# Kernel optimization log

Measured on AMD Instinct MI355X. Metric: run time of the kernel, lower is better.

## Reference

```python
import jax, jax.numpy as jnp
import numpy as np

EMBED = 256; HEADS = 8; LEVELS = 1; POINTS = 4; QUEUE = 2
HB = 200; WB = 200; NQ = HB * WB; BS = 1


def bilinear_sample(img, grid, h, w):
    # img: (BH, D, h*w) flattened feature map; grid: (BH, N, 2) in [-1, 1]
    # torch.grid_sample(align_corners=False, padding_mode='zeros') semantics
    gx, gy = grid[..., 0], grid[..., 1]
    x = (gx + 1.0) * (w * 0.5) - 0.5
    y = (gy + 1.0) * (h * 0.5) - 0.5
    x0 = jnp.floor(x); y0 = jnp.floor(y)
    lx = x - x0; ly = y - y0
    x0i = x0.astype(jnp.int32); y0i = y0.astype(jnp.int32)

    def corner(xi, yi, wgt):
        valid = ((xi >= 0) & (xi < w) & (yi >= 0) & (yi < h)).astype(img.dtype)
        idx = jnp.clip(yi, 0, h - 1) * w + jnp.clip(xi, 0, w - 1)  # (BH, N)
        vals = jax.vmap(lambda im, ix: im[:, ix])(img, idx)  # (BH, D, N)
        return vals * (wgt * valid)[:, None, :]

    return (corner(x0i, y0i, (1 - lx) * (1 - ly))
            + corner(x0i + 1, y0i, lx * (1 - ly))
            + corner(x0i, y0i + 1, (1 - lx) * ly)
            + corner(x0i + 1, y0i + 1, lx * ly))


def ms_deform_attn(value, shapes, loc, aw):
    # value: (B, Nv, H, D); loc: (B, nq, H, L, P, 2); aw: (B, nq, H, L, P)
    B, Nv, H, D = value.shape
    nq = loc.shape[1]; P = loc.shape[4]
    grids = 2.0 * loc - 1.0
    start = 0
    per_level = []
    for l in range(shapes.shape[0]):
        h, w = int(shapes[l, 0]), int(shapes[l, 1])
        vl = value[:, start:start + h * w].reshape(B, h, w, H, D)
        vl = vl.transpose(0, 3, 4, 1, 2).reshape(B * H, D, h * w)
        g = grids[:, :, :, l].transpose(0, 2, 1, 3, 4).reshape(B * H, nq * P, 2)
        samp = bilinear_sample(vl, g, h, w).reshape(B, H, D, nq, P)
        per_level.append(samp)
        start += h * w
    sampled = jnp.stack(per_level, axis=4)  # (B, H, D, nq, L, P)
    w_ = aw.transpose(0, 2, 1, 3, 4)[:, :, None]  # (B, H, 1, nq, L, P)
    out = (sampled * w_).sum(axis=(-1, -2))  # (B, H, D, nq)
    return out.reshape(B, H * D, nq).transpose(0, 2, 1)  # (B, nq, E)


def setup_inputs():
    key = jax.random.key(0)
    ks = jax.random.split(key, 10)
    s = 0.02
    n_off = QUEUE * HEADS * LEVELS * POINTS * 2
    n_aw = QUEUE * HEADS * LEVELS * POINTS
    return {
        "query": jax.random.normal(ks[0], (BS, NQ, EMBED), jnp.float32),
        "query_pos": jax.random.normal(ks[1], (BS, NQ, EMBED), jnp.float32),
        "value": jax.random.normal(ks[2], (BS * QUEUE, NQ, EMBED), jnp.float32),
        "reference_points": jax.random.uniform(ks[3], (BS * QUEUE, NQ, LEVELS, 2), jnp.float32),
        "spatial_shapes": jnp.array([[HB, WB]], dtype=jnp.int32),
        "W_off": jax.random.normal(ks[4], (EMBED * QUEUE, n_off), jnp.float32) * s,
        "b_off": jnp.zeros((n_off,), jnp.float32),
        "W_attn": jax.random.normal(ks[5], (EMBED * QUEUE, n_aw), jnp.float32) * s,
        "b_attn": jnp.zeros((n_aw,), jnp.float32),
        "W_val": jax.random.normal(ks[6], (EMBED, EMBED), jnp.float32) * s,
        "b_val": jnp.zeros((EMBED,), jnp.float32),
        "W_out": jax.random.normal(ks[7], (EMBED, EMBED), jnp.float32) * s,
        "b_out": jnp.zeros((EMBED,), jnp.float32),
    }


def reference(query, query_pos, value, reference_points, spatial_shapes,
              W_off, b_off, W_attn, b_attn, W_val, b_val, W_out, b_out):
    shapes = np.asarray(spatial_shapes)  # static level shapes
    bs, nq, E = query.shape
    identity = query
    q = query + query_pos
    # temporal query: concat current-frame value with query
    q2 = jnp.concatenate([value[:bs], q], axis=-1)  # (bs, nq, 2E)
    v = value @ W_val + b_val  # (bs*2, nv, E)
    nv = v.shape[1]
    v = v.reshape(bs * QUEUE, nv, HEADS, E // HEADS)
    off = (q2 @ W_off + b_off).reshape(bs, nq, HEADS, QUEUE, LEVELS, POINTS, 2)
    aw = (q2 @ W_attn + b_attn).reshape(bs, nq, HEADS, QUEUE, LEVELS * POINTS)
    aw = jax.nn.softmax(aw, axis=-1).reshape(bs, nq, HEADS, QUEUE, LEVELS, POINTS)
    aw = aw.transpose(0, 3, 1, 2, 4, 5).reshape(bs * QUEUE, nq, HEADS, LEVELS, POINTS)
    off = off.transpose(0, 3, 1, 2, 4, 5, 6).reshape(bs * QUEUE, nq, HEADS, LEVELS, POINTS, 2)
    # normalized sampling locations: (bs*2, nq, H, L, P, 2)
    normalizer = jnp.stack([spatial_shapes[..., 1], spatial_shapes[..., 0]], -1).astype(jnp.float32)
    loc = reference_points[:, :, None, :, None, :] + off / normalizer[None, None, None, :, None, :]
    out = ms_deform_attn(v, shapes, loc, aw)  # (bs*2, nq, E)
    # average over the BEV queue (current + history)
    out = out.transpose(1, 2, 0).reshape(nq, E, bs, QUEUE).mean(-1).transpose(2, 0, 1)
    out = out @ W_out + b_out
    return out + identity
```

## Files before the change

### kernel.cpp

```cpp
#include <hip/hip_runtime.h>
#include <math.h>

#define NQ    40000
#define EMB   256
#define NHEAD 8
#define HDIM  32
#define HB    200
#define WB    200
#define NCOL  192
#define HPIX  2560000

typedef __attribute__((ext_vector_type(8))) __bf16 bf16x8;
typedef __attribute__((ext_vector_type(4))) float f32x4;

static __device__ __forceinline__ unsigned short f2bf(float f) {
  unsigned u = __float_as_uint(f);
  u = u + 0x7fffu + ((u >> 16) & 1u);
  return (unsigned short)(u >> 16);
}
static __device__ __forceinline__ float bf2f(unsigned short s) {
  return __uint_as_float(((unsigned)s) << 16);
}
static __device__ __forceinline__ void accp(float4& lo4, float4& hi4, uint4 u, float w) {
  lo4.x += w * __uint_as_float(u.x << 16);
  lo4.y += w * __uint_as_float(u.x & 0xffff0000u);
  lo4.z += w * __uint_as_float(u.y << 16);
  lo4.w += w * __uint_as_float(u.y & 0xffff0000u);
  hi4.x += w * __uint_as_float(u.z << 16);
  hi4.y += w * __uint_as_float(u.z & 0xffff0000u);
  hi4.z += w * __uint_as_float(u.w << 16);
  hi4.w += w * __uint_as_float(u.w & 0xffff0000u);
}

__global__ __launch_bounds__(256) void conv_w(
    const float* __restrict__ W_off, const float* __restrict__ b_off,
    const float* __restrict__ W_attn, const float* __restrict__ b_attn,
    const float* __restrict__ W_val, const float* __restrict__ W_out,
    unsigned short* __restrict__ Wc1t, unsigned short* __restrict__ Wvt,
    unsigned short* __restrict__ Wot, float* __restrict__ bc1)
{
  int idx = blockIdx.x * 256 + threadIdx.x;
  if (idx < 65536) {
    int k = idx >> 7, n = idx & 127;
    Wc1t[(size_t)n * 512 + k] = f2bf(W_off[idx]);
  } else if (idx < 98304) {
    int j = idx - 65536;
    int k = j >> 6, n = j & 63;
    Wc1t[(size_t)(128 + n) * 512 + k] = f2bf(W_attn[j]);
  } else if (idx < 163840) {
    int j = idx - 98304;
    int k = j >> 8, n = j & 255;
    Wvt[(size_t)n * 256 + k] = f2bf(W_val[j]);
  } else if (idx < 229376) {
    int j = idx - 163840;
    int k = j >> 8, n = j & 255;
    Wot[(size_t)n * 256 + k] = f2bf(W_out[j]);
  } else if (idx < 229568) {
    int n = idx - 229376;
    bc1[n] = (n < 128) ? b_off[n] : b_attn[n - 128];
  }
}

template<int K, int N, int AMODE, int OMODE, bool RESID>
static __device__ __forceinline__ void gemm_body(
    int bx, char* lds,
    const void* __restrict__ Aptr, const void* __restrict__ Aq2a,
    const void* __restrict__ Aq2b, const unsigned short* __restrict__ Bt,
    const float* __restrict__ bias, const float* __restrict__ resid,
    void* __restrict__ outp)
{
  constexpr int NFR = N / 64;
  constexpr int NP  = N + 8;
  unsigned short* trn = (unsigned short*)lds;

  const int t = threadIdx.x;
  const int m0 = bx * 32;
  const int wid = t >> 6, lane = t & 63;
  const int wn = wid * (N / 4);
  const int lr = lane & 15, quad = lane >> 4;

  auto cvt_store = [&](int r, int c, float4 f0, float4 f1) {
    union { unsigned short us[8]; uint4 v; } u;
    u.us[0] = f2bf(f0.x); u.us[1] = f2bf(f0.y);
    u.us[2] = f2bf(f0.z); u.us[3] = f2bf(f0.w);
    u.us[4] = f2bf(f1.x); u.us[5] = f2bf(f1.y);
    u.us[6] = f2bf(f1.z); u.us[7] = f2bf(f1.w);
    *(uint4*)(lds + (size_t)r * 512 + ((c ^ (r & 7)) * 16)) = u.v;
  };

  auto stage_h = [&](int hh) {
    const int c = t & 31, r0 = t >> 5;
    if (AMODE == 1 || hh == 0) {
      float4 f[4][2];
      #pragma unroll
      for (int l = 0; l < 4; l++) {
        const float* s = (const float*)Aptr
            + (size_t)(m0 + r0 + 8 * l) * 256 + c * 8;
        f[l][0] = *(const float4*)s; f[l][1] = *(const float4*)(s + 4);
      }
      #pragma unroll
      for (int l = 0; l < 4; l++)
        cvt_store(r0 + 8 * l, c, f[l][0], f[l][1]);
    } else {
      float4 fq[4][2], fp[4][2];
      #pragma unroll
      for (int l = 0; l < 4; l++) {
        int row = m0 + r0 + 8 * l;
        const float* sq = (const float*)Aq2a + (size_t)row * 256 + c * 8;
        const float* sp = (const float*)Aq2b + (size_t)row * 256 + c * 8;
        fq[l][0] = *(const float4*)sq; fq[l][1] = *(const float4*)(sq + 4);
        fp[l][0] = *(const float4*)sp; fp[l][1] = *(const float4*)(sp + 4);
      }
      #pragma unroll
      for (int l = 0; l < 4; l++) {
        float4 f0 = make_float4(fq[l][0].x + fp[l][0].x, fq[l][0].y + fp[l][0].y,
                                fq[l][0].z + fp[l][0].z, fq[l][0].w + fp[l][0].w);
        float4 f1 = make_float4(fq[l][1].x + fp[l][1].x, fq[l][1].y + fp[l][1].y,
                                fq[l][1].z + fp[l][1].z, fq[l][1].w + fp[l][1].w);
        cvt_store(r0 + 8 * l, c, f0, f1);
      }
    }
  };

  f32x4 acc[2][NFR];
  #pragma unroll
  for (int i = 0; i < 2; i++)
    #pragma unroll
    for (int n = 0; n < NFR; n++) acc[i][n] = (f32x4){0.f, 0.f, 0.f, 0.f};

  auto loadB = [&](bf16x8* dst, int k0) {
    #pragma unroll
    for (int n = 0; n < NFR; n++)
      dst[n] = *(const bf16x8*)(Bt + (size_t)(wn + n * 16 + lr) * K + k0 + quad * 8);
  };
  auto loadA_lds = [&](bf16x8* dst, int lk) {
    const int cb = (lk >> 3) + quad;
    const int sw = (cb ^ (lr & 7)) * 16;
    #pragma unroll
    for (int i = 0; i < 2; i++)
      dst[i] = *(const bf16x8*)(lds + (size_t)(lr + i * 16) * 512 + sw);
  };
  auto loadA_dir = [&](bf16x8* dst, int k0) {
    if constexpr (AMODE == 0) {
      const unsigned short* A = (const unsigned short*)Aptr;
      #pragma unroll
      for (int i = 0; i < 2; i++)
        dst[i] = *(const bf16x8*)(A + (size_t)(m0 + lr + i * 16) * K + k0 + quad * 8);
    } else {
      const unsigned short* A = (const unsigned short*)Aptr;
      const int h = k0 >> 5;
      #pragma unroll
      for (int i = 0; i < 2; i++)
        dst[i] = *(const bf16x8*)(A + (size_t)h * NQ * 32
                                    + (size_t)(m0 + lr + i * 16) * 32 + quad * 8);
    }
  };

  if constexpr (AMODE == 1 || AMODE == 2) {
    constexpr int NH = K / 256;
    #pragma unroll
    for (int hh = 0; hh < NH; hh++) {
      if (hh) __syncthreads();
      stage_h(hh);
      __syncthreads();
      bf16x8 b0[NFR], b1[NFR], af[2];
      loadB(b0, hh * 256);
      loadB(b1, hh * 256 + 32);
      loadA_lds(af, 0);
      #pragma unroll
      for (int ks = 0; ks < 8; ks++) {
        bf16x8 b2[NFR], an[2];
        if (ks + 2 < 8) loadB(b2, hh * 256 + (ks + 2) * 32);
        if (ks + 1 < 8) loadA_lds(an, (ks + 1) * 32);
        #pragma unroll
        for (int i = 0; i < 2; i++)
          #pragma unroll
          for (int n = 0; n < NFR; n++)
            acc[i][n] = __builtin_amdgcn_mfma_f32_16x16x32_bf16(af[i], b0[n], acc[i][n], 0, 0, 0);
        #pragma unroll
        for (int n = 0; n < NFR; n++) { b0[n] = b1[n]; b1[n] = b2[n]; }
        af[0] = an[0]; af[1] = an[1];
      }
    }
  } else {
    constexpr int NK = K / 32;
    bf16x8 b0[NFR], b1[NFR], af[2];
    loadB(b0, 0);
    if (NK > 1) loadB(b1, 32);
    loadA_dir(af, 0);
    #pragma unroll
    for (int ks = 0; ks < NK; ks++) {
      bf16x8 b2[NFR], an[2];
      if (ks + 2 < NK) loadB(b2, (ks + 2) * 32);
      if (ks + 1 < NK) loadA_dir(an, (ks + 1) * 32);
      #pragma unroll
      for (int i = 0; i < 2; i++)
        #pragma unroll
        for (int n = 0; n < NFR; n++)
          acc[i][n] = __builtin_amdgcn_mfma_f32_16x16x32_bf16(af[i], b0[n], acc[i][n], 0, 0, 0);
      #pragma unroll
      for (int n = 0; n < NFR; n++) { b0[n] = b1[n]; b1[n] = b2[n]; }
      af[0] = an[0]; af[1] = an[1];
    }
  }

  if constexpr (OMODE == 0) {
    #pragma unroll
    for (int i = 0; i < 2; i++) {
      int rowb = m0 + i * 16 + quad * 4;
      #pragma unroll
      for (int n = 0; n < NFR; n++) {
        int col = wn + n * 16 + lr;
        float bsv = bias[col];
        #pragma unroll
        for (int r = 0; r < 4; r++) {
          int rr = rowb + r;
          float v = acc[i][n][r] + bsv;
          if (RESID) v += resid[(size_t)rr * N + col];
          ((float*)outp)[(size_t)rr * N + col] = v;
        }
      }
    }
  } else {
    __syncthreads();
    #pragma unroll
    for (int i = 0; i < 2; i++) {
      #pragma unroll
      for (int n = 0; n < NFR; n++) {
        int col = wn + n * 16 + lr;
        float bsv = bias[col];
        #pragma unroll
        for (int r = 0; r < 4; r++) {
          int rl = i * 16 + quad * 4 + r;
          trn[rl * NP + col] = f2bf(acc[i][n][r] + bsv);
        }
      }
    }
    __syncthreads();
    constexpr int NCH = (32 * N) / 2048;
    #pragma unroll
    for (int l = 0; l < NCH; l++) {
      int c = t + l * 256;
      int row = c / (N / 8);
      int coloff = (c % (N / 8)) * 8;
      uint4 d = *(const uint4*)(trn + row * NP + coloff);
      unsigned short* op = (unsigned short*)outp;
      if constexpr (OMODE == 2)
        op += (size_t)(coloff >> 5) * HPIX + (size_t)(m0 + row) * 32 + (coloff & 31);
      else
        op += (size_t)(m0 + row) * N + coloff;
      *(uint4*)op = d;
    }
  }
}

__global__ __launch_bounds__(256, 4) void k12(
    const float* __restrict__ value, const float* __restrict__ query,
    const float* __restrict__ qpos, const unsigned short* __restrict__ Wc1t,
    const unsigned short* __restrict__ Wvt, const float* __restrict__ bc1,
    const float* __restrict__ b_val, unsigned short* __restrict__ raw1,
    unsigned short* __restrict__ vout)
{
  __shared__ __align__(16) char lds[16896];
  const int bx = blockIdx.x;
  if (bx < 1250) {
    gemm_body<512, 192, 2, 1, false>(bx, lds, value, query, qpos,
                                     Wc1t, bc1, nullptr, raw1);
  } else {
    gemm_body<256, 256, 1, 2, false>(bx - 1250, lds, value, nullptr, nullptr,
                                     Wvt, b_val, nullptr, vout);
  }
}

__global__ __launch_bounds__(256, 4) void k4g(
    const unsigned short* __restrict__ msd, const unsigned short* __restrict__ Wot,
    const float* __restrict__ b_out, const float* __restrict__ query,
    float* __restrict__ out)
{
  __shared__ __align__(16) char lds[64];
  gemm_body<256, 256, 4, 0, true>(blockIdx.x, lds, msd, nullptr, nullptr,
                                  Wot, b_out, query, out);
}

__global__ __launch_bounds__(256) void k3_sample(
    const unsigned short* __restrict__ raw1, const float* __restrict__ refp,
    const unsigned short* __restrict__ vh, unsigned short* __restrict__ msd)
{
  __shared__ int4   sidx[512];
  __shared__ float4 swgt[512];
  const int t = threadIdx.x;
  const int h  = blockIdx.x & 7;
  const int q0 = (blockIdx.x >> 3) * 64;

  #pragma unroll
  for (int ee = 0; ee < 2; ee++) {
    const int e = t + ee * 256;
    const int qi = e >> 3, b = (e >> 2) & 1, p = e & 3;
    const int q = q0 + qi;
    const unsigned short* r = raw1 + (size_t)q * NCOL;
    float ox = bf2f(r[h * 16 + b * 8 + p * 2 + 0]);
    float oy = bf2f(r[h * 16 + b * 8 + p * 2 + 1]);
    float l0 = bf2f(r[128 + h * 8 + b * 4 + 0]);
    float l1 = bf2f(r[128 + h * 8 + b * 4 + 1]);
    float l2 = bf2f(r[128 + h * 8 + b * 4 + 2]);
    float l3 = bf2f(r[128 + h * 8 + b * 4 + 3]);
    float mx = fmaxf(fmaxf(l0, l1), fmaxf(l2, l3));
    float e0 = expf(l0 - mx), e1 = expf(l1 - mx);
    float e2 = expf(l2 - mx), e3 = expf(l3 - mx);
    float ssum = e0 + e1 + e2 + e3;
    float ep = (p == 0) ? e0 : (p == 1) ? e1 : (p == 2) ? e2 : e3;
    float aw = ep / ssum * 0.5f;
    float rx = refp[((size_t)b * NQ + q) * 2 + 0];
    float ry = refp[((size_t)b * NQ + q) * 2 + 1];
    float px = rx * (float)WB + ox - 0.5f;
    float py = ry * (float)HB + oy - 0.5f;
    float x0f = floorf(px), y0f = floorf(py);
    float lx = px - x0f, ly = py - y0f;
    int x0 = (int)x0f, y0 = (int)y0f, x1 = x0 + 1, y1 = y0 + 1;
    int x0c = min(max(x0, 0), WB - 1), x1c = min(max(x1, 0), WB - 1);
    int y0c = min(max(y0, 0), HB - 1), y1c = min(max(y1, 0), HB - 1);
    float vx0 = ((unsigned)x0 < (unsigned)WB) ? 1.f : 0.f;
    float vx1 = ((unsigned)x1 < (unsigned)WB) ? 1.f : 0.f;
    float vy0 = ((unsigned)y0 < (unsigned)HB) ? 1.f : 0.f;
    float vy1 = ((unsigned)y1 < (unsigned)HB) ? 1.f : 0.f;
    const int pb = b * NQ;
    int4 ix;
    ix.x = pb + y0c * WB + x0c;
    ix.y = pb + y0c * WB + x1c;
    ix.z = pb + y1c * WB + x0c;
    ix.w = pb + y1c * WB + x1c;
    float4 wv;
    wv.x = aw * (1.f - lx) * (1.f - ly) * vx0 * vy0;
    wv.y = aw * lx * (1.f - ly) * vx1 * vy0;
    wv.z = aw * (1.f - lx) * ly * vx0 * vy1;
    wv.w = aw * lx * ly * vx1 * vy1;
    sidx[e] = ix;
    swgt[e] = wv;
  }
  __syncthreads();

  const int qi = t >> 2, c = t & 3;
  const unsigned short* vb = vh + (size_t)h * HPIX + c * 8;
  float4 lo = {0.f, 0.f, 0.f, 0.f}, hi = lo;
  #pragma unroll
  for (int b = 0; b < 2; b++) {
    #pragma unroll
    for (int p = 0; p < 4; p++) {
      int ent = qi * 8 + b * 4 + p;
      int4 pix = sidx[ent];
      float4 wv = swgt[ent];
      accp(lo, hi, *(const uint4*)(vb + (size_t)pix.x * 32), wv.x);
      accp(lo, hi, *(const uint4*)(vb + (size_t)pix.y * 32), wv.y);
      accp(lo, hi, *(const uint4*)(vb + (size_t)pix.z * 32), wv.z);
      accp(lo, hi, *(const uint4*)(vb + (size_t)pix.w * 32), wv.w);
    }
  }
  union { unsigned short us[8]; uint4 v; } o;
  o.us[0] = f2bf(lo.x); o.us[1] = f2bf(lo.y);
  o.us[2] = f2bf(lo.z); o.us[3] = f2bf(lo.w);
  o.us[4] = f2bf(hi.x); o.us[5] = f2bf(hi.y);
  o.us[6] = f2bf(hi.z); o.us[7] = f2bf(hi.w);
  *(uint4*)(msd + (size_t)h * NQ * 32 + (size_t)(q0 + qi) * 32 + c * 8) = o.v;
}

extern "C" void kernel_launch(void* const* d_in, const int* in_sizes, int n_in,
                              void* d_out, int out_size, void* d_ws, size_t ws_size,
                              hipStream_t stream) {
  const float* query     = (const float*)d_in[0];
  const float* query_pos = (const float*)d_in[1];
  const float* value     = (const float*)d_in[2];
  const float* refp      = (const float*)d_in[3];
  const float* W_off  = (const float*)d_in[5];
  const float* b_off  = (const float*)d_in[6];
  const float* W_attn = (const float*)d_in[7];
  const float* b_attn = (const float*)d_in[8];
  const float* W_val  = (const float*)d_in[9];
  const float* b_val  = (const float*)d_in[10];
  const float* W_out  = (const float*)d_in[11];
  const float* b_out  = (const float*)d_in[12];
  float* out = (float*)d_out;

  char* ws = (char*)d_ws;
  unsigned short* raw1 = (unsigned short*)(ws);
  unsigned short* vout = (unsigned short*)(ws + 15360000);
  unsigned short* msdb = (unsigned short*)(ws + 56320000);
  unsigned short* Wc1t = (unsigned short*)(ws + 76800000);
  unsigned short* Wvt  = (unsigned short*)(ws + 76996608);
  unsigned short* Wot  = (unsigned short*)(ws + 77127680);
  float*          bc1  = (float*)(ws + 77258752);

  hipLaunchKernelGGL(conv_w, dim3(897), dim3(256), 0, stream,
                     W_off, b_off, W_attn, b_attn, W_val, W_out, Wc1t, Wvt, Wot, bc1);

  hipLaunchKernelGGL(k12, dim3(3750), dim3(256), 0, stream,
                     value, query, query_pos, Wc1t, Wvt, bc1, b_val, raw1, vout);

  hipLaunchKernelGGL(k3_sample, dim3(5000), dim3(256), 0, stream,
                     raw1, refp, vout, msdb);

  hipLaunchKernelGGL(k4g, dim3(1250), dim3(256), 0, stream,
                     msdb, Wot, b_out, query, out);
}
```

Baseline: 337.1 us.

## Fuse all stages into persistent megakernel with atomic grid barriers

Replaces the four separate kernel launches (weight conversion, projection GEMMs, deformable sampling, output GEMM) with one persistent kernel of 1280 blocks. The blocks loop over each stage's tiles and wait at software grid barriers built on an atomic counter, which is reset by a memset before the launch. The aim is to remove launch gaps and kernel-boundary drain between stages. In exchange, all stages share one LDS allocation and one launch-bounds setting, tail imbalance inside each stage remains, and the barrier relies on all 1280 blocks being co-resident or it deadlocks.

```diff
diff --git a/kernel.cpp b/kernel.cpp
--- a/kernel.cpp
+++ b/kernel.cpp
@@ -9,6 +9,7 @@
 #define WB    200
 #define NCOL  192
 #define HPIX  2560000
+#define GRID  1280
 
 typedef __attribute__((ext_vector_type(8))) __bf16 bf16x8;
 typedef __attribute__((ext_vector_type(4))) float f32x4;
@@ -32,14 +33,27 @@
   hi4.w += w * __uint_as_float(u.w & 0xffff0000u);
 }
 
-__global__ __launch_bounds__(256) void conv_w(
+static __device__ __forceinline__ void grid_sync(unsigned* bar) {
+  __syncthreads();
+  if (threadIdx.x == 0) {
+    __threadfence();
+    unsigned my = atomicAdd(bar, 1u) + 1u;
+    unsigned tgt = ((my - 1u) / (unsigned)GRID + 1u) * (unsigned)GRID;
+    while (atomicAdd(bar, 0u) < tgt) { __builtin_amdgcn_s_sleep(16); }
+    __threadfence();
+  }
+  __syncthreads();
+}
+
+static __device__ __forceinline__ void conv_body(
+    int tile, int t,
     const float* __restrict__ W_off, const float* __restrict__ b_off,
     const float* __restrict__ W_attn, const float* __restrict__ b_attn,
     const float* __restrict__ W_val, const float* __restrict__ W_out,
     unsigned short* __restrict__ Wc1t, unsigned short* __restrict__ Wvt,
     unsigned short* __restrict__ Wot, float* __restrict__ bc1)
 {
-  int idx = blockIdx.x * 256 + threadIdx.x;
+  int idx = tile * 256 + t;
   if (idx < 65536) {
     int k = idx >> 7, n = idx & 127;
     Wc1t[(size_t)n * 512 + k] = f2bf(W_off[idx]);
@@ -254,43 +268,16 @@
   }
 }
 
-__global__ __launch_bounds__(256, 4) void k12(
-    const float* __restrict__ value, const float* __restrict__ query,
-    const float* __restrict__ qpos, const unsigned short* __restrict__ Wc1t,
-    const unsigned short* __restrict__ Wvt, const float* __restrict__ bc1,
-    const float* __restrict__ b_val, unsigned short* __restrict__ raw1,
-    unsigned short* __restrict__ vout)
-{
-  __shared__ __align__(16) char lds[16896];
-  const int bx = blockIdx.x;
-  if (bx < 1250) {
-    gemm_body<512, 192, 2, 1, false>(bx, lds, value, query, qpos,
-                                     Wc1t, bc1, nullptr, raw1);
-  } else {
-    gemm_body<256, 256, 1, 2, false>(bx - 1250, lds, value, nullptr, nullptr,
-                                     Wvt, b_val, nullptr, vout);
-  }
-}
-
-__global__ __launch_bounds__(256, 4) void k4g(
-    const unsigned short* __restrict__ msd, const unsigned short* __restrict__ Wot,
-    const float* __restrict__ b_out, const float* __restrict__ query,
-    float* __restrict__ out)
-{
-  __shared__ __align__(16) char lds[64];
-  gemm_body<256, 256, 4, 0, true>(blockIdx.x, lds, msd, nullptr, nullptr,
-                                  Wot, b_out, query, out);
-}
-
-__global__ __launch_bounds__(256) void k3_sample(
+static __device__ __forceinline__ void k3_body(
+    int tile, char* lds,
     const unsigned short* __restrict__ raw1, const float* __restrict__ refp,
     const unsigned short* __restrict__ vh, unsigned short* __restrict__ msd)
 {
-  __shared__ int4   sidx[512];
-  __shared__ float4 swgt[512];
+  int4*   sidx = (int4*)lds;
+  float4* swgt = (float4*)(lds + 8192);
   const int t = threadIdx.x;
-  const int h  = blockIdx.x & 7;
-  const int q0 = (blockIdx.x >> 3) * 64;
+  const int h  = tile & 7;
+  const int q0 = (tile >> 3) * 64;
 
   #pragma unroll
   for (int ee = 0; ee < 2; ee++) {
@@ -363,6 +350,49 @@
   *(uint4*)(msd + (size_t)h * NQ * 32 + (size_t)(q0 + qi) * 32 + c * 8) = o.v;
 }
 
+__global__ __launch_bounds__(256, 8) void mega(
+    const float* __restrict__ value, const float* __restrict__ query,
+    const float* __restrict__ qpos, const float* __restrict__ refp,
+    const float* __restrict__ W_off, const float* __restrict__ b_off,
+    const float* __restrict__ W_attn, const float* __restrict__ b_attn,
+    const float* __restrict__ W_val, const float* __restrict__ b_val,
+    const float* __restrict__ W_out, const float* __restrict__ b_out,
+    unsigned short* __restrict__ raw1, unsigned short* __restrict__ vout,
+    unsigned short* __restrict__ msdb, unsigned short* __restrict__ Wc1t,
+    unsigned short* __restrict__ Wvt, unsigned short* __restrict__ Wot,
+    float* __restrict__ bc1, float* __restrict__ out, unsigned* bar)
+{
+  __shared__ __align__(16) char lds[16896];
+  const int bid = blockIdx.x;
+  const int t = threadIdx.x;
+
+  for (int tile = bid; tile < 897; tile += GRID)
+    conv_body(tile, t, W_off, b_off, W_attn, b_attn, W_val, W_out,
+              Wc1t, Wvt, Wot, bc1);
+  grid_sync(bar);
+
+  for (int tile = bid; tile < 3750; tile += GRID) {
+    if (tile < 1250)
+      gemm_body<512, 192, 2, 1, false>(tile, lds, value, query, qpos,
+                                       Wc1t, bc1, nullptr, raw1);
+    else
+      gemm_body<256, 256, 1, 2, false>(tile - 1250, lds, value, nullptr,
+                                       nullptr, Wvt, b_val, nullptr, vout);
+    __syncthreads();
+  }
+  grid_sync(bar);
+
+  for (int tile = bid; tile < 5000; tile += GRID) {
+    k3_body(tile, lds, raw1, refp, vout, msdb);
+    __syncthreads();
+  }
+  grid_sync(bar);
+
+  for (int tile = bid; tile < 1250; tile += GRID)
+    gemm_body<256, 256, 4, 0, true>(tile, lds, msdb, nullptr, nullptr,
+                                    Wot, b_out, query, out);
+}
+
 extern "C" void kernel_launch(void* const* d_in, const int* in_sizes, int n_in,
                               void* d_out, int out_size, void* d_ws, size_t ws_size,
                               hipStream_t stream) {
@@ -388,16 +418,12 @@
   unsigned short* Wvt  = (unsigned short*)(ws + 76996608);
   unsigned short* Wot  = (unsigned short*)(ws + 77127680);
   float*          bc1  = (float*)(ws + 77258752);
-
-  hipLaunchKernelGGL(conv_w, dim3(897), dim3(256), 0, stream,
-                     W_off, b_off, W_attn, b_attn, W_val, W_out, Wc1t, Wvt, Wot, bc1);
-
-  hipLaunchKernelGGL(k12, dim3(3750), dim3(256), 0, stream,
-                     value, query, query_pos, Wc1t, Wvt, bc1, b_val, raw1, vout);
-
-  hipLaunchKernelGGL(k3_sample, dim3(5000), dim3(256), 0, stream,
-                     raw1, refp, vout, msdb);
-
-  hipLaunchKernelGGL(k4g, dim3(1250), dim3(256), 0, stream,
-                     msdb, Wot, b_out, query, out);
-}
+  unsigned*       bar  = (unsigned*)(ws + 77259520);
+
+  hipMemsetAsync(bar, 0, 4, stream);
+
+  hipLaunchKernelGGL(mega, dim3(GRID), dim3(256), 0, stream,
+                     value, query, query_pos, refp,
+                     W_off, b_off, W_attn, b_attn, W_val, b_val, W_out, b_out,
+                     raw1, vout, msdb, Wc1t, Wvt, Wot, bc1, out, bar);
+}
```

Result: slower. 1.202 ms (+256.7%).
